# Kernel optimization log

Measured on AMD Instinct MI355X. Metric: run time of the kernel, lower is better.

## Reference

```python
import jax, jax.numpy as jnp
import numpy as np

K, N, D = 128, 512, 256
THETA = 784.0
BATCH = 16384


def _expm_np(M):
    # scaling-and-squaring Taylor expm in float64 numpy (deterministic, no scipy)
    nrm = np.linalg.norm(M, 1)
    s = max(0, int(np.ceil(np.log2(max(nrm, 1.0)))) + 1)
    A = M / (2.0 ** s)
    E = np.eye(M.shape[0])
    term = np.eye(M.shape[0])
    for i in range(1, 30):
        term = term @ A / i
        E = E + term
    for _ in range(s):
        E = E @ E
    return E


def _legendre_zoh(theta, order):
    Q = np.arange(order, dtype=np.float64)
    R = (2 * Q + 1)[:, None] / theta
    j, i = np.meshgrid(Q, Q)
    A = np.where(i < j, -1.0, (-1.0) ** (i - j + 1)) * R
    B = (-1.0) ** Q[:, None] * R
    # ZOH discretization with dt=1: expm([[A, B], [0, 0]])
    M = np.zeros((order + 1, order + 1))
    M[:order, :order] = A
    M[:order, order:] = B
    E = _expm_np(M)
    return E[:order, :order], E[:order, order:]  # Ad (d,d), Bd (d,1)


def setup_inputs() -> dict:
    key = jax.random.key(0)
    ks = jax.random.split(key, 9)
    x = jax.random.normal(ks[0], (BATCH, K), dtype=jnp.float32)
    h = jax.random.normal(ks[1], (BATCH, N), dtype=jnp.float32)
    m = jax.random.normal(ks[2], (BATCH, D), dtype=jnp.float32)
    # xavier-normal-ish weights
    Wx = jax.random.normal(ks[3], (N, K), dtype=jnp.float32) * np.sqrt(2.0 / (N + K))
    Wh = jax.random.normal(ks[4], (N, N), dtype=jnp.float32) * np.sqrt(2.0 / (N + N))
    Wm = jax.random.normal(ks[5], (N, D), dtype=jnp.float32) * np.sqrt(2.0 / (N + D))
    lim = np.sqrt(3.0 / D)
    ex = jax.random.uniform(ks[6], (1, K), dtype=jnp.float32, minval=-lim, maxval=lim)
    eh = jax.random.uniform(ks[7], (1, N), dtype=jnp.float32, minval=-lim, maxval=lim)
    em = jnp.zeros((1, D), dtype=jnp.float32)
    Ad, Bd = _legendre_zoh(THETA, D)
    AT = jnp.asarray(Ad, dtype=jnp.float32)  # (d, d)
    BT = jnp.asarray(Bd, dtype=jnp.float32)  # (d, 1)
    return {"x": x, "h": h, "m": m, "Wx": Wx, "Wh": Wh, "Wm": Wm,
            "ex": ex, "eh": eh, "em": em, "AT": AT, "BT": BT}


def reference(x, h, m, Wx, Wh, Wm, ex, eh, em, AT, BT):
    # u: (B, 1) scalar input signal per batch element
    u = x @ ex.T + h @ eh.T + m @ em.T
    # memory update: m' = m A^T + u B^T  -> (B, d)
    new_m = m @ AT.T + u @ BT.T
    # hidden update: h' = sigmoid(x Wx^T + h Wh^T + m' Wm^T)
    new_h = jax.nn.sigmoid(x @ Wx.T + h @ Wh.T + new_m @ Wm.T)
    return (new_h, new_m)
```

## Files before the change

kernel.cpp:

```cpp
#include <hip/hip_runtime.h>


typedef __bf16 bf16;
typedef bf16  bf16x8 __attribute__((ext_vector_type(8)));
typedef float f32x4  __attribute__((ext_vector_type(4)));
typedef unsigned short u16;

#define BATCH 16384
#define WPACK 0
#define ATPACK 458752
#define WUOFF 524288
#define UOFF  525312
#define APACK 558080

#define PACK_ITEMS 393728
#define PACK_BLOCKS 1538
#define WM2_BLOCKS 128

__device__ __forceinline__ u16 f2bf(float f) {
  unsigned u = __builtin_bit_cast(unsigned, f);
  u += 0x7FFFu + ((u >> 16) & 1u);
  return (u16)(u >> 16);
}

__device__ __forceinline__ void gload16(const u16* g, u16* l) {
  __builtin_amdgcn_global_load_lds(
      (const __attribute__((address_space(1))) unsigned int*)g,
      (__attribute__((address_space(3))) unsigned int*)l, 16, 0, 0);
}

__global__ __launch_bounds__(256) void lmu_wpack(
    const float* __restrict__ Wx, const float* __restrict__ Wh,
    const float* __restrict__ Wm, const float* __restrict__ AT,
    const float* __restrict__ BT, u16* __restrict__ ws) {
  __shared__ float wmt[16 * 256];
  const int bx = blockIdx.x;
  if (bx < PACK_BLOCKS) {
    int i = bx * 256 + threadIdx.x;
    if (i < 327680) {
      int j = i & 7, rest = i >> 3;
      int n = rest & 511, kk = rest >> 9;
      int k = kk * 8 + j;
      float v = (k < 128) ? Wx[n * 128 + k] : Wh[n * 512 + (k - 128)];
      ws[WPACK + i] = f2bf(v);
    } else if (i < 393216) {
      int t = i - 327680;
      int j = t & 7, rest = t >> 3;
      int d = rest & 255, kk = rest >> 8;
      ws[ATPACK + t] = f2bf(AT[d * 256 + kk * 8 + j]);
    } else if (i < PACK_ITEMS) {
      int n = i - 393216;
      float s = 0.f;
      for (int k = 0; k < 256; k += 4) {
        float4 wv = *(const float4*)(Wm + (size_t)n * 256 + k);
        float4 bv = *(const float4*)(BT + k);
        s += wv.x * bv.x + wv.y * bv.y + wv.z * bv.z + wv.w * bv.w;
      }
      ((float*)(ws + WUOFF))[n] = s;
    }
  } else {
    const int wq = bx - PACK_BLOCKS;
    const int t = threadIdx.x;
    const int nb = (wq & 31) * 16, db = (wq >> 5) * 64;
#pragma unroll
    for (int it = 0; it < 4; ++it) {
      int f = it * 256 + t;
      float4 v = *(const float4*)(Wm + (size_t)(nb + (f >> 6)) * 256 + (f & 63) * 4);
      *(float4*)(wmt + (f >> 6) * 256 + (f & 63) * 4) = v;
    }
    __syncthreads();
    const int d = db + (t & 63);
    const int nn = (t >> 6) * 4;
    float acc[4] = {0.f, 0.f, 0.f, 0.f};
    for (int k = 0; k < 256; ++k) {
      float atv = AT[(size_t)k * 256 + d];
#pragma unroll
      for (int i2 = 0; i2 < 4; ++i2) acc[i2] += wmt[(nn + i2) * 256 + k] * atv;
    }
    const int kk = 80 + (d >> 3), j = d & 7;
#pragma unroll
    for (int i2 = 0; i2 < 4; ++i2)
      ws[WPACK + ((size_t)kk * 512 + (nb + nn + i2)) * 8 + j] = f2bf(acc[i2]);
  }
}

__global__ __launch_bounds__(256) void lmu_prep(
    const float* __restrict__ x, const float* __restrict__ h,
    const float* __restrict__ m, const float* __restrict__ ex,
    const float* __restrict__ eh, const float* __restrict__ em,
    u16* __restrict__ ws) {
  const int lane = threadIdx.x & 63;
  const int row  = blockIdx.x * 4 + (threadIdx.x >> 6);
  u16* ap = ws + APACK + (size_t)row * 896;
  float s = 0.f;
#pragma unroll
  for (int j = 0; j < 4; ++j) {
    int slot = j * 64 + lane;
    if (slot < 224) {
      float4 a, e;
      if (slot < 32)       { int c = slot * 4;
        a = *(const float4*)(x + (size_t)row * 128 + c); e = *(const float4*)(ex + c); }
      else if (slot < 160) { int c = (slot - 32) * 4;
        a = *(const float4*)(h + (size_t)row * 512 + c); e = *(const float4*)(eh + c); }
      else                 { int c = (slot - 160) * 4;
        a = *(const float4*)(m + (size_t)row * 256 + c); e = *(const float4*)(em + c); }
      s += a.x * e.x + a.y * e.y + a.z * e.z + a.w * e.w;
      unsigned long long pk =
          (unsigned long long)f2bf(a.x)
        | ((unsigned long long)f2bf(a.y) << 16)
        | ((unsigned long long)f2bf(a.z) << 32)
        | ((unsigned long long)f2bf(a.w) << 48);
      *(unsigned long long*)(ap + slot * 4) = pk;
    }
  }
#pragma unroll
  for (int d = 1; d < 64; d <<= 1) s += __shfl_xor(s, d);
  if (lane == 0) ((float*)(ws + UOFF))[row] = s;
}

__global__ __launch_bounds__(512, 4) void lmu_gemm(
    const u16* __restrict__ ws, const float* __restrict__ BT,
    float* __restrict__ out) {
  __shared__ __align__(16) u16 smem[2 * 20480];
  const int tid  = threadIdx.x;
  const int lane = tid & 63;
  const int w    = tid >> 6;
  const int wr   = w >> 1;
  const int wc   = w & 1;
  const int lm   = lane & 15;
  const int kg   = lane >> 4;
  const int bid  = blockIdx.x;
  const int mi   = (bid & 7) | ((bid >> 5) << 3);
  const int nsl  = (bid >> 3) & 3;
  const int b0   = mi * 128;

  const u16* apack = ws + APACK;
  const u16* wpk   = ws + WPACK;
  const u16* atp   = ws + ATPACK;

  f32x4 acc[2][4];
  f32x4 acc2[2][2];
#pragma unroll
  for (int mt = 0; mt < 2; ++mt) {
#pragma unroll
    for (int ct = 0; ct < 4; ++ct) acc[mt][ct] = (f32x4){0.f, 0.f, 0.f, 0.f};
#pragma unroll
    for (int ct = 0; ct < 2; ++ct) acc2[mt][ct] = (f32x4){0.f, 0.f, 0.f, 0.f};
  }

  auto stage = [&](int c) {
    u16* buf = smem + (c & 1) * 20480;
#pragma unroll
    for (int ph = 0; ph < 2; ++ph) {
      int i = ph * 512 + tid;
      int kb = i >> 7, r = i & 127;
      gload16(apack + (size_t)(b0 + r) * 896 + c * 64 + kb * 8, buf + i * 8);
    }
#pragma unroll
    for (int ph = 0; ph < 2; ++ph) {
      int i = ph * 512 + tid;
      int kk = i >> 7, n = i & 127;
      gload16(wpk + ((size_t)(c * 8 + kk) * 512 + nsl * 128 + n) * 8,
              buf + 8192 + i * 8);
    }
    if (c >= 10) {
      int kk = tid >> 6, n = tid & 63;
      gload16(atp + ((size_t)((c - 10) * 8 + kk) * 256 + nsl * 64 + n) * 8,
              buf + 16384 + tid * 8);
    }
  };

  auto mma = [&](int c) {
    const u16* buf = smem + (c & 1) * 20480;
#pragma unroll
    for (int ks = 0; ks < 2; ++ks) {
      const int kq = ks * 4 + kg;
      bf16x8 a[2];
#pragma unroll
      for (int mt = 0; mt < 2; ++mt)
        a[mt] = *(const bf16x8*)(buf + (kq * 128 + wr * 32 + mt * 16 + lm) * 8);
#pragma unroll
      for (int ct = 0; ct < 4; ++ct) {
        bf16x8 b = *(const bf16x8*)(buf + 8192 + (kq * 128 + wc * 64 + ct * 16 + lm) * 8);
#pragma unroll
        for (int mt = 0; mt < 2; ++mt)
          acc[mt][ct] = __builtin_amdgcn_mfma_f32_16x16x32_bf16(a[mt], b, acc[mt][ct], 0, 0, 0);
      }
      if (c >= 10) {
#pragma unroll
        for (int ct = 0; ct < 2; ++ct) {
          bf16x8 b = *(const bf16x8*)(buf + 16384 + (kq * 64 + wc * 32 + ct * 16 + lm) * 8);
#pragma unroll
          for (int mt = 0; mt < 2; ++mt)
            acc2[mt][ct] = __builtin_amdgcn_mfma_f32_16x16x32_bf16(a[mt], b, acc2[mt][ct], 0, 0, 0);
        }
      }
    }
  };

  stage(0);
  __syncthreads();
#pragma unroll
  for (int c = 0; c < 14; ++c) {
    if (c < 13) stage(c + 1);
    mma(c);
    __syncthreads();
  }

  const float* uf  = (const float*)(ws + UOFF);
  const float* wuf = (const float*)(ws + WUOFF);
  float wuv[4], btv[2];
#pragma unroll
  for (int ct = 0; ct < 4; ++ct) wuv[ct] = wuf[nsl * 128 + wc * 64 + ct * 16 + lm];
#pragma unroll
  for (int ct = 0; ct < 2; ++ct) btv[ct] = BT[nsl * 64 + wc * 32 + ct * 16 + lm];
  float* outm = out + (size_t)BATCH * 512;
#pragma unroll
  for (int mt = 0; mt < 2; ++mt)
#pragma unroll
    for (int j = 0; j < 4; ++j) {
      int rl = wr * 32 + mt * 16 + kg * 4 + j;
      size_t row = (size_t)(b0 + rl);
      float uv = uf[row];
#pragma unroll
      for (int ct = 0; ct < 4; ++ct) {
        float v = acc[mt][ct][j] + uv * wuv[ct];
        out[row * 512 + nsl * 128 + wc * 64 + ct * 16 + lm] = 1.0f / (1.0f + __expf(-v));
      }
#pragma unroll
      for (int ct = 0; ct < 2; ++ct)
        outm[row * 256 + nsl * 64 + wc * 32 + ct * 16 + lm] = acc2[mt][ct][j] + uv * btv[ct];
    }
}

extern "C" void kernel_launch(void* const* d_in, const int* in_sizes, int n_in,
                              void* d_out, int out_size, void* d_ws, size_t ws_size,
                              hipStream_t stream) {
  const float* x  = (const float*)d_in[0];
  const float* h  = (const float*)d_in[1];
  const float* m  = (const float*)d_in[2];
  const float* Wx = (const float*)d_in[3];
  const float* Wh = (const float*)d_in[4];
  const float* Wm = (const float*)d_in[5];
  const float* ex = (const float*)d_in[6];
  const float* eh = (const float*)d_in[7];
  const float* em = (const float*)d_in[8];
  const float* AT = (const float*)d_in[9];
  const float* BT = (const float*)d_in[10];
  float* out = (float*)d_out;
  u16* ws = (u16*)d_ws;

  lmu_wpack<<<PACK_BLOCKS + WM2_BLOCKS, 256, 0, stream>>>(Wx, Wh, Wm, AT, BT, ws);
  lmu_prep<<<BATCH / 4, 256, 0, stream>>>(x, h, m, ex, eh, em, ws);
  lmu_gemm<<<512, 512, 0, stream>>>(ws, BT, out);
}
```

Before: 61.58 us.

## Merge prep kernels and use triple-buffered K-loop with vmcnt waits

The weight-packing and activation-prep kernels become one launch, which removes a kernel boundary. The GEMM K-step is halved to 32, and the loop now runs a three-buffer LDS ring with a prefetch distance of two. It waits with explicit s_waitcnt vmcnt counts and raw s_barrier instead of __syncthreads, so global loads overlap compute more and each block uses less LDS. The risks are more barriers per block and fragile manual vmcnt accounting, since the AT loads appear partway through the loop.

```diff
diff --git a/kernel.cpp b/kernel.cpp
--- a/kernel.cpp
+++ b/kernel.cpp
@@ -16,6 +16,7 @@
 #define PACK_ITEMS 393728
 #define PACK_BLOCKS 1538
 #define WM2_BLOCKS 128
+#define PREP_BLOCKS 4096
 
 __device__ __forceinline__ u16 f2bf(float f) {
   unsigned u = __builtin_bit_cast(unsigned, f);
@@ -29,10 +30,13 @@
       (__attribute__((address_space(3))) unsigned int*)l, 16, 0, 0);
 }
 
-__global__ __launch_bounds__(256) void lmu_wpack(
+__global__ __launch_bounds__(256) void lmu_pre(
     const float* __restrict__ Wx, const float* __restrict__ Wh,
     const float* __restrict__ Wm, const float* __restrict__ AT,
-    const float* __restrict__ BT, u16* __restrict__ ws) {
+    const float* __restrict__ BT, const float* __restrict__ x,
+    const float* __restrict__ h, const float* __restrict__ m,
+    const float* __restrict__ ex, const float* __restrict__ eh,
+    const float* __restrict__ em, u16* __restrict__ ws) {
   __shared__ float wmt[16 * 256];
   const int bx = blockIdx.x;
   if (bx < PACK_BLOCKS) {
@@ -58,7 +62,7 @@
       }
       ((float*)(ws + WUOFF))[n] = s;
     }
-  } else {
+  } else if (bx < PACK_BLOCKS + WM2_BLOCKS) {
     const int wq = bx - PACK_BLOCKS;
     const int t = threadIdx.x;
     const int nb = (wq & 31) * 16, db = (wq >> 5) * 64;
@@ -81,47 +85,41 @@
 #pragma unroll
     for (int i2 = 0; i2 < 4; ++i2)
       ws[WPACK + ((size_t)kk * 512 + (nb + nn + i2)) * 8 + j] = f2bf(acc[i2]);
+  } else {
+    const int lane = threadIdx.x & 63;
+    const int row  = (bx - PACK_BLOCKS - WM2_BLOCKS) * 4 + (threadIdx.x >> 6);
+    u16* ap = ws + APACK + (size_t)row * 896;
+    float s = 0.f;
+#pragma unroll
+    for (int j = 0; j < 4; ++j) {
+      int slot = j * 64 + lane;
+      if (slot < 224) {
+        float4 a, e;
+        if (slot < 32)       { int c = slot * 4;
+          a = *(const float4*)(x + (size_t)row * 128 + c); e = *(const float4*)(ex + c); }
+        else if (slot < 160) { int c = (slot - 32) * 4;
+          a = *(const float4*)(h + (size_t)row * 512 + c); e = *(const float4*)(eh + c); }
+        else                 { int c = (slot - 160) * 4;
+          a = *(const float4*)(m + (size_t)row * 256 + c); e = *(const float4*)(em + c); }
+        s += a.x * e.x + a.y * e.y + a.z * e.z + a.w * e.w;
+        unsigned long long pk =
+            (unsigned long long)f2bf(a.x)
+          | ((unsigned long long)f2bf(a.y) << 16)
+          | ((unsigned long long)f2bf(a.z) << 32)
+          | ((unsigned long long)f2bf(a.w) << 48);
+        *(unsigned long long*)(ap + slot * 4) = pk;
+      }
+    }
+#pragma unroll
+    for (int d = 1; d < 64; d <<= 1) s += __shfl_xor(s, d);
+    if (lane == 0) ((float*)(ws + UOFF))[row] = s;
   }
-}
-
-__global__ __launch_bounds__(256) void lmu_prep(
-    const float* __restrict__ x, const float* __restrict__ h,
-    const float* __restrict__ m, const float* __restrict__ ex,
-    const float* __restrict__ eh, const float* __restrict__ em,
-    u16* __restrict__ ws) {
-  const int lane = threadIdx.x & 63;
-  const int row  = blockIdx.x * 4 + (threadIdx.x >> 6);
-  u16* ap = ws + APACK + (size_t)row * 896;
-  float s = 0.f;
-#pragma unroll
-  for (int j = 0; j < 4; ++j) {
-    int slot = j * 64 + lane;
-    if (slot < 224) {
-      float4 a, e;
-      if (slot < 32)       { int c = slot * 4;
-        a = *(const float4*)(x + (size_t)row * 128 + c); e = *(const float4*)(ex + c); }
-      else if (slot < 160) { int c = (slot - 32) * 4;
-        a = *(const float4*)(h + (size_t)row * 512 + c); e = *(const float4*)(eh + c); }
-      else                 { int c = (slot - 160) * 4;
-        a = *(const float4*)(m + (size_t)row * 256 + c); e = *(const float4*)(em + c); }
-      s += a.x * e.x + a.y * e.y + a.z * e.z + a.w * e.w;
-      unsigned long long pk =
-          (unsigned long long)f2bf(a.x)
-        | ((unsigned long long)f2bf(a.y) << 16)
-        | ((unsigned long long)f2bf(a.z) << 32)
-        | ((unsigned long long)f2bf(a.w) << 48);
-      *(unsigned long long*)(ap + slot * 4) = pk;
-    }
-  }
-#pragma unroll
-  for (int d = 1; d < 64; d <<= 1) s += __shfl_xor(s, d);
-  if (lane == 0) ((float*)(ws + UOFF))[row] = s;
 }
 
 __global__ __launch_bounds__(512, 4) void lmu_gemm(
     const u16* __restrict__ ws, const float* __restrict__ BT,
     float* __restrict__ out) {
-  __shared__ __align__(16) u16 smem[2 * 20480];
+  __shared__ __align__(16) u16 smem[36864];
   const int tid  = threadIdx.x;
   const int lane = tid & 63;
   const int w    = tid >> 6;
@@ -137,6 +135,14 @@
   const u16* apack = ws + APACK;
   const u16* wpk   = ws + WPACK;
   const u16* atp   = ws + ATPACK;
+  const float* uf  = (const float*)(ws + UOFF);
+  const float* wuf = (const float*)(ws + WUOFF);
+
+  float wuv[4], btv[2];
+#pragma unroll
+  for (int ct = 0; ct < 4; ++ct) wuv[ct] = wuf[nsl * 128 + wc * 64 + ct * 16 + lm];
+#pragma unroll
+  for (int ct = 0; ct < 2; ++ct) btv[ct] = BT[nsl * 64 + wc * 32 + ct * 16 + lm];
 
   f32x4 acc[2][4];
   f32x4 acc2[2][2];
@@ -148,72 +154,63 @@
     for (int ct = 0; ct < 2; ++ct) acc2[mt][ct] = (f32x4){0.f, 0.f, 0.f, 0.f};
   }
 
-  auto stage = [&](int c) {
-    u16* buf = smem + (c & 1) * 20480;
-#pragma unroll
-    for (int ph = 0; ph < 2; ++ph) {
-      int i = ph * 512 + tid;
-      int kb = i >> 7, r = i & 127;
-      gload16(apack + (size_t)(b0 + r) * 896 + c * 64 + kb * 8, buf + i * 8);
-    }
-#pragma unroll
-    for (int ph = 0; ph < 2; ++ph) {
-      int i = ph * 512 + tid;
-      int kk = i >> 7, n = i & 127;
-      gload16(wpk + ((size_t)(c * 8 + kk) * 512 + nsl * 128 + n) * 8,
-              buf + 8192 + i * 8);
-    }
-    if (c >= 10) {
-      int kk = tid >> 6, n = tid & 63;
-      gload16(atp + ((size_t)((c - 10) * 8 + kk) * 256 + nsl * 64 + n) * 8,
-              buf + 16384 + tid * 8);
+  auto stage = [&](int c, u16* buf) {
+    gload16(apack + (size_t)(b0 + (tid & 127)) * 896 + c * 32 + (tid >> 7) * 8,
+            buf + tid * 8);
+    gload16(wpk + ((size_t)(c * 4 + (tid >> 7)) * 512 + nsl * 128 + (tid & 127)) * 8,
+            buf + 4096 + tid * 8);
+    if (c >= 20) {
+      int cm = c - 20;
+      gload16(atp + ((size_t)(cm * 4 + (tid >> 7)) * 256 + nsl * 64 + (tid & 63)) * 8,
+              buf + 8192 + tid * 8);
     }
   };
 
-  auto mma = [&](int c) {
-    const u16* buf = smem + (c & 1) * 20480;
-#pragma unroll
-    for (int ks = 0; ks < 2; ++ks) {
-      const int kq = ks * 4 + kg;
-      bf16x8 a[2];
-#pragma unroll
-      for (int mt = 0; mt < 2; ++mt)
-        a[mt] = *(const bf16x8*)(buf + (kq * 128 + wr * 32 + mt * 16 + lm) * 8);
-#pragma unroll
-      for (int ct = 0; ct < 4; ++ct) {
-        bf16x8 b = *(const bf16x8*)(buf + 8192 + (kq * 128 + wc * 64 + ct * 16 + lm) * 8);
+  auto mma = [&](const u16* buf, int c) {
+    const int kq = kg;
+    bf16x8 a[2], b[4];
+#pragma unroll
+    for (int mt = 0; mt < 2; ++mt)
+      a[mt] = *(const bf16x8*)(buf + (kq * 128 + wr * 32 + mt * 16 + lm) * 8);
+#pragma unroll
+    for (int ct = 0; ct < 4; ++ct)
+      b[ct] = *(const bf16x8*)(buf + 4096 + (kq * 128 + wc * 64 + ct * 16 + lm) * 8);
+#pragma unroll
+    for (int mt = 0; mt < 2; ++mt)
+#pragma unroll
+      for (int ct = 0; ct < 4; ++ct)
+        acc[mt][ct] = __builtin_amdgcn_mfma_f32_16x16x32_bf16(a[mt], b[ct], acc[mt][ct], 0, 0, 0);
+    if (c >= 20) {
+#pragma unroll
+      for (int ct = 0; ct < 2; ++ct) {
+        bf16x8 s = *(const bf16x8*)(buf + 8192 + (kq * 128 + wc * 32 + ct * 16 + lm) * 8);
 #pragma unroll
         for (int mt = 0; mt < 2; ++mt)
-          acc[mt][ct] = __builtin_amdgcn_mfma_f32_16x16x32_bf16(a[mt], b, acc[mt][ct], 0, 0, 0);
-      }
-      if (c >= 10) {
-#pragma unroll
-        for (int ct = 0; ct < 2; ++ct) {
-          bf16x8 b = *(const bf16x8*)(buf + 16384 + (kq * 64 + wc * 32 + ct * 16 + lm) * 8);
-#pragma unroll
-          for (int mt = 0; mt < 2; ++mt)
-            acc2[mt][ct] = __builtin_amdgcn_mfma_f32_16x16x32_bf16(a[mt], b, acc2[mt][ct], 0, 0, 0);
-        }
+          acc2[mt][ct] = __builtin_amdgcn_mfma_f32_16x16x32_bf16(a[mt], s, acc2[mt][ct], 0, 0, 0);
       }
     }
   };
 
-  stage(0);
-  __syncthreads();
-#pragma unroll
-  for (int c = 0; c < 14; ++c) {
-    if (c < 13) stage(c + 1);
-    mma(c);
-    __syncthreads();
+  u16 *p0 = smem, *p1 = smem + 12288, *p2 = smem + 24576;
+
+  stage(0, p0);
+  stage(1, p1);
+  asm volatile("s_waitcnt vmcnt(2)" ::: "memory");
+  __builtin_amdgcn_s_barrier();
+
+#pragma unroll 1
+  for (int c = 0; c < 28; ++c) {
+    if (c + 2 < 28) stage(c + 2, p2);
+    mma(p0, c);
+    if (c < 27) {
+      if (c < 18)      asm volatile("s_waitcnt vmcnt(2)" ::: "memory");
+      else if (c < 26) asm volatile("s_waitcnt vmcnt(3)" ::: "memory");
+      else             asm volatile("s_waitcnt vmcnt(0)" ::: "memory");
+      __builtin_amdgcn_s_barrier();
+    }
+    u16* t0 = p0; p0 = p1; p1 = p2; p2 = t0;
   }
 
-  const float* uf  = (const float*)(ws + UOFF);
-  const float* wuf = (const float*)(ws + WUOFF);
-  float wuv[4], btv[2];
-#pragma unroll
-  for (int ct = 0; ct < 4; ++ct) wuv[ct] = wuf[nsl * 128 + wc * 64 + ct * 16 + lm];
-#pragma unroll
-  for (int ct = 0; ct < 2; ++ct) btv[ct] = BT[nsl * 64 + wc * 32 + ct * 16 + lm];
   float* outm = out + (size_t)BATCH * 512;
 #pragma unroll
   for (int mt = 0; mt < 2; ++mt)
@@ -250,7 +247,7 @@
   float* out = (float*)d_out;
   u16* ws = (u16*)d_ws;
 
-  lmu_wpack<<<PACK_BLOCKS + WM2_BLOCKS, 256, 0, stream>>>(Wx, Wh, Wm, AT, BT, ws);
-  lmu_prep<<<BATCH / 4, 256, 0, stream>>>(x, h, m, ex, eh, em, ws);
+  lmu_pre<<<PACK_BLOCKS + WM2_BLOCKS + PREP_BLOCKS, 256, 0, stream>>>(
+      Wx, Wh, Wm, AT, BT, x, h, m, ex, eh, em, ws);
   lmu_gemm<<<512, 512, 0, stream>>>(ws, BT, out);
 }
```

Result: faster. 53.04 us (-13.9%).

## Merge weight packing and activation prep into one kernel with k-major A layout

Applied to the files above, without the earlier changes.

Fuses the weight-packing kernel and the activation bf16-conversion kernel into a single 512-thread launch, removing one kernel launch and letting both kinds of work run concurrently. The activation pack moves from row-major to k-chunk-major (kk, batch, 8) order and is transposed through an XOR-swizzled LDS tile before being written out. The GEMM's A-tile loads then read contiguous 16-byte chunks across rows, which should coalesce better. In exchange, the prep blocks carry a large 56 KB shared allocation that lowers occupancy for every block in the merged kernel, and bf16 conversion now uses the native cast instead of manual rounding.

```diff
diff --git a/kernel.cpp b/kernel.cpp
--- a/kernel.cpp
+++ b/kernel.cpp
@@ -2,6 +2,7 @@
 
 
 typedef __bf16 bf16;
+typedef bf16  bf16x4 __attribute__((ext_vector_type(4)));
 typedef bf16  bf16x8 __attribute__((ext_vector_type(8)));
 typedef float f32x4  __attribute__((ext_vector_type(4)));
 typedef unsigned short u16;
@@ -14,8 +15,9 @@
 #define APACK 558080
 
 #define PACK_ITEMS 393728
-#define PACK_BLOCKS 1538
+#define PACKA_BLOCKS 769
 #define WM2_BLOCKS 128
+#define PREP_BLOCKS 512
 
 __device__ __forceinline__ u16 f2bf(float f) {
   unsigned u = __builtin_bit_cast(unsigned, f);
@@ -29,14 +31,18 @@
       (__attribute__((address_space(3))) unsigned int*)l, 16, 0, 0);
 }
 
-__global__ __launch_bounds__(256) void lmu_wpack(
+__global__ __launch_bounds__(512) void lmu_pre(
     const float* __restrict__ Wx, const float* __restrict__ Wh,
     const float* __restrict__ Wm, const float* __restrict__ AT,
-    const float* __restrict__ BT, u16* __restrict__ ws) {
-  __shared__ float wmt[16 * 256];
+    const float* __restrict__ BT, const float* __restrict__ x,
+    const float* __restrict__ h, const float* __restrict__ m,
+    const float* __restrict__ ex, const float* __restrict__ eh,
+    const float* __restrict__ em, u16* __restrict__ ws) {
+  __shared__ __align__(16) char psm[57344];
   const int bx = blockIdx.x;
-  if (bx < PACK_BLOCKS) {
-    int i = bx * 256 + threadIdx.x;
+  const int t  = threadIdx.x;
+  if (bx < PACKA_BLOCKS) {
+    int i = bx * 512 + t;
     if (i < 327680) {
       int j = i & 7, rest = i >> 3;
       int n = rest & 511, kk = rest >> 9;
@@ -44,11 +50,11 @@
       float v = (k < 128) ? Wx[n * 128 + k] : Wh[n * 512 + (k - 128)];
       ws[WPACK + i] = f2bf(v);
     } else if (i < 393216) {
-      int t = i - 327680;
-      int j = t & 7, rest = t >> 3;
+      int tt = i - 327680;
+      int j = tt & 7, rest = tt >> 3;
       int d = rest & 255, kk = rest >> 8;
-      ws[ATPACK + t] = f2bf(AT[d * 256 + kk * 8 + j]);
-    } else if (i < PACK_ITEMS) {
+      ws[ATPACK + tt] = f2bf(AT[d * 256 + kk * 8 + j]);
+    } else {
       int n = i - 393216;
       float s = 0.f;
       for (int k = 0; k < 256; k += 4) {
@@ -58,64 +64,70 @@
       }
       ((float*)(ws + WUOFF))[n] = s;
     }
-  } else {
-    const int wq = bx - PACK_BLOCKS;
-    const int t = threadIdx.x;
+  } else if (bx < PACKA_BLOCKS + WM2_BLOCKS) {
+    float* wmt = (float*)psm;
+    const int wq = bx - PACKA_BLOCKS;
     const int nb = (wq & 31) * 16, db = (wq >> 5) * 64;
 #pragma unroll
-    for (int it = 0; it < 4; ++it) {
-      int f = it * 256 + t;
+    for (int it = 0; it < 2; ++it) {
+      int f = it * 512 + t;
       float4 v = *(const float4*)(Wm + (size_t)(nb + (f >> 6)) * 256 + (f & 63) * 4);
       *(float4*)(wmt + (f >> 6) * 256 + (f & 63) * 4) = v;
     }
     __syncthreads();
     const int d = db + (t & 63);
-    const int nn = (t >> 6) * 4;
-    float acc[4] = {0.f, 0.f, 0.f, 0.f};
+    const int nn = (t >> 6) * 2;
+    float acc[2] = {0.f, 0.f};
     for (int k = 0; k < 256; ++k) {
       float atv = AT[(size_t)k * 256 + d];
 #pragma unroll
-      for (int i2 = 0; i2 < 4; ++i2) acc[i2] += wmt[(nn + i2) * 256 + k] * atv;
+      for (int i2 = 0; i2 < 2; ++i2) acc[i2] += wmt[(nn + i2) * 256 + k] * atv;
     }
     const int kk = 80 + (d >> 3), j = d & 7;
 #pragma unroll
-    for (int i2 = 0; i2 < 4; ++i2)
+    for (int i2 = 0; i2 < 2; ++i2)
       ws[WPACK + ((size_t)kk * 512 + (nb + nn + i2)) * 8 + j] = f2bf(acc[i2]);
+  } else {
+    const int px   = bx - PACKA_BLOCKS - WM2_BLOCKS;
+    const int lane = t & 63;
+    const int wv   = t >> 6;
+    float* uo = (float*)(ws + UOFF);
+    u16* ap = ws + APACK;
+#pragma unroll
+    for (int rr = 0; rr < 4; ++rr) {
+      const int rl = wv * 4 + rr;
+      const size_t rg = (size_t)px * 32 + rl;
+      float s = 0.f;
+#pragma unroll
+      for (int j = 0; j < 4; ++j) {
+        int slot = j * 64 + lane;
+        if (slot < 224) {
+          float4 a, e;
+          if (slot < 32)       { int c = slot * 4;
+            a = *(const float4*)(x + rg * 128 + c); e = *(const float4*)(ex + c); }
+          else if (slot < 160) { int c = (slot - 32) * 4;
+            a = *(const float4*)(h + rg * 512 + c); e = *(const float4*)(eh + c); }
+          else                 { int c = (slot - 160) * 4;
+            a = *(const float4*)(m + rg * 256 + c); e = *(const float4*)(em + c); }
+          s += a.x * e.x + a.y * e.y + a.z * e.z + a.w * e.w;
+          bf16x4 p = {(bf16)a.x, (bf16)a.y, (bf16)a.z, (bf16)a.w};
+          int kk = slot >> 1, hf = slot & 1;
+          *(bf16x4*)(psm + rl * 1792 + ((kk ^ (rl & 7)) << 4) + hf * 8) = p;
+        }
+      }
+#pragma unroll
+      for (int d = 1; d < 64; d <<= 1) s += __shfl_xor(s, d);
+      if (lane == 0) uo[rg] = s;
+    }
+    __syncthreads();
+#pragma unroll
+    for (int it = 0; it < 7; ++it) {
+      int flat = it * 512 + t;
+      int kk = flat >> 5, r = flat & 31;
+      bf16x8 v = *(const bf16x8*)(psm + r * 1792 + ((kk ^ (r & 7)) << 4));
+      *(bf16x8*)(ap + ((size_t)kk * BATCH + (size_t)px * 32 + r) * 8) = v;
+    }
   }
-}
-
-__global__ __launch_bounds__(256) void lmu_prep(
-    const float* __restrict__ x, const float* __restrict__ h,
-    const float* __restrict__ m, const float* __restrict__ ex,
-    const float* __restrict__ eh, const float* __restrict__ em,
-    u16* __restrict__ ws) {
-  const int lane = threadIdx.x & 63;
-  const int row  = blockIdx.x * 4 + (threadIdx.x >> 6);
-  u16* ap = ws + APACK + (size_t)row * 896;
-  float s = 0.f;
-#pragma unroll
-  for (int j = 0; j < 4; ++j) {
-    int slot = j * 64 + lane;
-    if (slot < 224) {
-      float4 a, e;
-      if (slot < 32)       { int c = slot * 4;
-        a = *(const float4*)(x + (size_t)row * 128 + c); e = *(const float4*)(ex + c); }
-      else if (slot < 160) { int c = (slot - 32) * 4;
-        a = *(const float4*)(h + (size_t)row * 512 + c); e = *(const float4*)(eh + c); }
-      else                 { int c = (slot - 160) * 4;
-        a = *(const float4*)(m + (size_t)row * 256 + c); e = *(const float4*)(em + c); }
-      s += a.x * e.x + a.y * e.y + a.z * e.z + a.w * e.w;
-      unsigned long long pk =
-          (unsigned long long)f2bf(a.x)
-        | ((unsigned long long)f2bf(a.y) << 16)
-        | ((unsigned long long)f2bf(a.z) << 32)
-        | ((unsigned long long)f2bf(a.w) << 48);
-      *(unsigned long long*)(ap + slot * 4) = pk;
-    }
-  }
-#pragma unroll
-  for (int d = 1; d < 64; d <<= 1) s += __shfl_xor(s, d);
-  if (lane == 0) ((float*)(ws + UOFF))[row] = s;
 }
 
 __global__ __launch_bounds__(512, 4) void lmu_gemm(
@@ -154,7 +166,7 @@
     for (int ph = 0; ph < 2; ++ph) {
       int i = ph * 512 + tid;
       int kb = i >> 7, r = i & 127;
-      gload16(apack + (size_t)(b0 + r) * 896 + c * 64 + kb * 8, buf + i * 8);
+      gload16(apack + ((size_t)(c * 8 + kb) * BATCH + b0 + r) * 8, buf + i * 8);
     }
 #pragma unroll
     for (int ph = 0; ph < 2; ++ph) {
@@ -250,7 +262,7 @@
   float* out = (float*)d_out;
   u16* ws = (u16*)d_ws;
 
-  lmu_wpack<<<PACK_BLOCKS + WM2_BLOCKS, 256, 0, stream>>>(Wx, Wh, Wm, AT, BT, ws);
-  lmu_prep<<<BATCH / 4, 256, 0, stream>>>(x, h, m, ex, eh, em, ws);
+  lmu_pre<<<PACKA_BLOCKS + WM2_BLOCKS + PREP_BLOCKS, 512, 0, stream>>>(
+      Wx, Wh, Wm, AT, BT, x, h, m, ex, eh, em, ws);
   lmu_gemm<<<512, 512, 0, stream>>>(ws, BT, out);
 }
```

Measured after the change: 53.98 us. 1.14x faster.

## Merge weight-pack and activation-prep kernels; reorder K chunks to store new_m early

Applied to the files above, without the earlier changes.

Folds the activation packing kernel into the weight-packing kernel as extra blocks, removing one kernel launch and the serialization between the two. In the GEMM, the K-chunk order is permuted so the m-part (shared with the AT product) is processed first. The new_m output is then written after chunk 4, overlapping those stores with the remaining MMA work instead of leaving them all for the epilogue. The u and wu values are loaded into registers up front, which adds some register pressure.

```diff
diff --git a/kernel.cpp b/kernel.cpp
--- a/kernel.cpp
+++ b/kernel.cpp
@@ -16,6 +16,7 @@
 #define PACK_ITEMS 393728
 #define PACK_BLOCKS 1538
 #define WM2_BLOCKS 128
+#define PREP_BLOCKS 4096
 
 __device__ __forceinline__ u16 f2bf(float f) {
   unsigned u = __builtin_bit_cast(unsigned, f);
@@ -29,10 +30,13 @@
       (__attribute__((address_space(3))) unsigned int*)l, 16, 0, 0);
 }
 
-__global__ __launch_bounds__(256) void lmu_wpack(
+__global__ __launch_bounds__(256) void lmu_pre(
     const float* __restrict__ Wx, const float* __restrict__ Wh,
     const float* __restrict__ Wm, const float* __restrict__ AT,
-    const float* __restrict__ BT, u16* __restrict__ ws) {
+    const float* __restrict__ BT, const float* __restrict__ x,
+    const float* __restrict__ h, const float* __restrict__ m,
+    const float* __restrict__ ex, const float* __restrict__ eh,
+    const float* __restrict__ em, u16* __restrict__ ws) {
   __shared__ float wmt[16 * 256];
   const int bx = blockIdx.x;
   if (bx < PACK_BLOCKS) {
@@ -58,7 +62,7 @@
       }
       ((float*)(ws + WUOFF))[n] = s;
     }
-  } else {
+  } else if (bx < PACK_BLOCKS + WM2_BLOCKS) {
     const int wq = bx - PACK_BLOCKS;
     const int t = threadIdx.x;
     const int nb = (wq & 31) * 16, db = (wq >> 5) * 64;
@@ -81,41 +85,39 @@
 #pragma unroll
     for (int i2 = 0; i2 < 4; ++i2)
       ws[WPACK + ((size_t)kk * 512 + (nb + nn + i2)) * 8 + j] = f2bf(acc[i2]);
+  } else {
+    const int lane = threadIdx.x & 63;
+    const int row  = (bx - PACK_BLOCKS - WM2_BLOCKS) * 4 + (threadIdx.x >> 6);
+    u16* ap = ws + APACK + (size_t)row * 896;
+    float s = 0.f;
+#pragma unroll
+    for (int j = 0; j < 4; ++j) {
+      int slot = j * 64 + lane;
+      if (slot < 224) {
+        float4 a, e;
+        if (slot < 32)       { int c = slot * 4;
+          a = *(const float4*)(x + (size_t)row * 128 + c); e = *(const float4*)(ex + c); }
+        else if (slot < 160) { int c = (slot - 32) * 4;
+          a = *(const float4*)(h + (size_t)row * 512 + c); e = *(const float4*)(eh + c); }
+        else                 { int c = (slot - 160) * 4;
+          a = *(const float4*)(m + (size_t)row * 256 + c); e = *(const float4*)(em + c); }
+        s += a.x * e.x + a.y * e.y + a.z * e.z + a.w * e.w;
+        unsigned long long pk =
+            (unsigned long long)f2bf(a.x)
+          | ((unsigned long long)f2bf(a.y) << 16)
+          | ((unsigned long long)f2bf(a.z) << 32)
+          | ((unsigned long long)f2bf(a.w) << 48);
+        *(unsigned long long*)(ap + slot * 4) = pk;
+      }
+    }
+#pragma unroll
+    for (int d = 1; d < 64; d <<= 1) s += __shfl_xor(s, d);
+    if (lane == 0) ((float*)(ws + UOFF))[row] = s;
   }
 }
 
-__global__ __launch_bounds__(256) void lmu_prep(
-    const float* __restrict__ x, const float* __restrict__ h,
-    const float* __restrict__ m, const float* __restrict__ ex,
-    const float* __restrict__ eh, const float* __restrict__ em,
-    u16* __restrict__ ws) {
-  const int lane = threadIdx.x & 63;
-  const int row  = blockIdx.x * 4 + (threadIdx.x >> 6);
-  u16* ap = ws + APACK + (size_t)row * 896;
-  float s = 0.f;
-#pragma unroll
-  for (int j = 0; j < 4; ++j) {
-    int slot = j * 64 + lane;
-    if (slot < 224) {
-      float4 a, e;
-      if (slot < 32)       { int c = slot * 4;
-        a = *(const float4*)(x + (size_t)row * 128 + c); e = *(const float4*)(ex + c); }
-      else if (slot < 160) { int c = (slot - 32) * 4;
-        a = *(const float4*)(h + (size_t)row * 512 + c); e = *(const float4*)(eh + c); }
-      else                 { int c = (slot - 160) * 4;
-        a = *(const float4*)(m + (size_t)row * 256 + c); e = *(const float4*)(em + c); }
-      s += a.x * e.x + a.y * e.y + a.z * e.z + a.w * e.w;
-      unsigned long long pk =
-          (unsigned long long)f2bf(a.x)
-        | ((unsigned long long)f2bf(a.y) << 16)
-        | ((unsigned long long)f2bf(a.z) << 32)
-        | ((unsigned long long)f2bf(a.w) << 48);
-      *(unsigned long long*)(ap + slot * 4) = pk;
-    }
-  }
-#pragma unroll
-  for (int d = 1; d < 64; d <<= 1) s += __shfl_xor(s, d);
-  if (lane == 0) ((float*)(ws + UOFF))[row] = s;
+__device__ __forceinline__ int koff_of(int c) {
+  return (c < 4) ? (640 + c * 64) : (c < 6) ? ((c - 4) * 64) : (128 + (c - 6) * 64);
 }
 
 __global__ __launch_bounds__(512, 4) void lmu_gemm(
@@ -137,6 +139,20 @@
   const u16* apack = ws + APACK;
   const u16* wpk   = ws + WPACK;
   const u16* atp   = ws + ATPACK;
+  const float* uf  = (const float*)(ws + UOFF);
+  const float* wuf = (const float*)(ws + WUOFF);
+  float* outm = out + (size_t)BATCH * 512;
+
+  float wuv[4], btv[2], ureg[2][4];
+#pragma unroll
+  for (int ct = 0; ct < 4; ++ct) wuv[ct] = wuf[nsl * 128 + wc * 64 + ct * 16 + lm];
+#pragma unroll
+  for (int ct = 0; ct < 2; ++ct) btv[ct] = BT[nsl * 64 + wc * 32 + ct * 16 + lm];
+#pragma unroll
+  for (int mt = 0; mt < 2; ++mt)
+#pragma unroll
+    for (int j = 0; j < 4; ++j)
+      ureg[mt][j] = uf[b0 + wr * 32 + mt * 16 + kg * 4 + j];
 
   f32x4 acc[2][4];
   f32x4 acc2[2][2];
@@ -150,22 +166,23 @@
 
   auto stage = [&](int c) {
     u16* buf = smem + (c & 1) * 20480;
+    const int ko = koff_of(c);
 #pragma unroll
     for (int ph = 0; ph < 2; ++ph) {
       int i = ph * 512 + tid;
       int kb = i >> 7, r = i & 127;
-      gload16(apack + (size_t)(b0 + r) * 896 + c * 64 + kb * 8, buf + i * 8);
+      gload16(apack + (size_t)(b0 + r) * 896 + ko + kb * 8, buf + i * 8);
     }
 #pragma unroll
     for (int ph = 0; ph < 2; ++ph) {
       int i = ph * 512 + tid;
       int kk = i >> 7, n = i & 127;
-      gload16(wpk + ((size_t)(c * 8 + kk) * 512 + nsl * 128 + n) * 8,
+      gload16(wpk + ((size_t)(ko / 8 + kk) * 512 + nsl * 128 + n) * 8,
               buf + 8192 + i * 8);
     }
-    if (c >= 10) {
+    if (c < 4) {
       int kk = tid >> 6, n = tid & 63;
-      gload16(atp + ((size_t)((c - 10) * 8 + kk) * 256 + nsl * 64 + n) * 8,
+      gload16(atp + ((size_t)(c * 8 + kk) * 256 + nsl * 64 + n) * 8,
               buf + 16384 + tid * 8);
     }
   };
@@ -186,7 +203,7 @@
         for (int mt = 0; mt < 2; ++mt)
           acc[mt][ct] = __builtin_amdgcn_mfma_f32_16x16x32_bf16(a[mt], b, acc[mt][ct], 0, 0, 0);
       }
-      if (c >= 10) {
+      if (c < 4) {
 #pragma unroll
         for (int ct = 0; ct < 2; ++ct) {
           bf16x8 b = *(const bf16x8*)(buf + 16384 + (kq * 64 + wc * 32 + ct * 16 + lm) * 8);
@@ -202,34 +219,36 @@
   __syncthreads();
 #pragma unroll
   for (int c = 0; c < 14; ++c) {
+    if (c == 4) {
+#pragma unroll
+      for (int mt = 0; mt < 2; ++mt)
+#pragma unroll
+        for (int j = 0; j < 4; ++j) {
+          int rl = wr * 32 + mt * 16 + kg * 4 + j;
+          size_t row = (size_t)(b0 + rl);
+#pragma unroll
+          for (int ct = 0; ct < 2; ++ct)
+            outm[row * 256 + nsl * 64 + wc * 32 + ct * 16 + lm] =
+                acc2[mt][ct][j] + ureg[mt][j] * btv[ct];
+        }
+    }
     if (c < 13) stage(c + 1);
     mma(c);
     __syncthreads();
   }
 
-  const float* uf  = (const float*)(ws + UOFF);
-  const float* wuf = (const float*)(ws + WUOFF);
-  float wuv[4], btv[2];
-#pragma unroll
-  for (int ct = 0; ct < 4; ++ct) wuv[ct] = wuf[nsl * 128 + wc * 64 + ct * 16 + lm];
-#pragma unroll
-  for (int ct = 0; ct < 2; ++ct) btv[ct] = BT[nsl * 64 + wc * 32 + ct * 16 + lm];
-  float* outm = out + (size_t)BATCH * 512;
 #pragma unroll
   for (int mt = 0; mt < 2; ++mt)
 #pragma unroll
     for (int j = 0; j < 4; ++j) {
       int rl = wr * 32 + mt * 16 + kg * 4 + j;
       size_t row = (size_t)(b0 + rl);
-      float uv = uf[row];
+      float uv = ureg[mt][j];
 #pragma unroll
       for (int ct = 0; ct < 4; ++ct) {
         float v = acc[mt][ct][j] + uv * wuv[ct];
         out[row * 512 + nsl * 128 + wc * 64 + ct * 16 + lm] = 1.0f / (1.0f + __expf(-v));
       }
-#pragma unroll
-      for (int ct = 0; ct < 2; ++ct)
-        outm[row * 256 + nsl * 64 + wc * 32 + ct * 16 + lm] = acc2[mt][ct][j] + uv * btv[ct];
     }
 }
 
@@ -250,7 +269,7 @@
   float* out = (float*)d_out;
   u16* ws = (u16*)d_ws;
 
-  lmu_wpack<<<PACK_BLOCKS + WM2_BLOCKS, 256, 0, stream>>>(Wx, Wh, Wm, AT, BT, ws);
-  lmu_prep<<<BATCH / 4, 256, 0, stream>>>(x, h, m, ex, eh, em, ws);
+  lmu_pre<<<PACK_BLOCKS + WM2_BLOCKS + PREP_BLOCKS, 256, 0, stream>>>(
+      Wx, Wh, Wm, AT, BT, x, h, m, ex, eh, em, ws);
   lmu_gemm<<<512, 512, 0, stream>>>(ws, BT, out);
 }
```

After: 53.82 us. 12.6% less time.
